# Optimization experiments

Hardware: AMD Instinct MI355X
Metric: run time of the kernel (lower is better)

The kernel has to match this reference:

```python
import jax, jax.numpy as jnp
import numpy as np

N_PER_GRAPH = 1000   # nodes per graph block (shape of A)
N_GRAPHS = 100       # number of block-diagonal replicas
N = N_PER_GRAPH * N_GRAPHS  # total nodes = 100000
HIDDEN = 128
DEG = 8
E = N * DEG          # total edges = 800000
LN_EPS = 1e-5


def setup_inputs() -> dict:
    key = jax.random.key(0)
    kx, kr, kc, kw, kb = jax.random.split(key, 5)
    # x rows: [S(N); I(N); R(N); params(N)] with beta in col0, gamma in col1
    x = jax.random.normal(kx, (4 * N, HIDDEN), dtype=jnp.float32)
    # block-diagonal COO edges: indices within each graph offset by graph id * n
    offs = jnp.repeat(jnp.arange(N_GRAPHS, dtype=jnp.int64) * N_PER_GRAPH,
                      N_PER_GRAPH * DEG)
    edge_row = offs + jax.random.randint(kr, (E,), 0, N_PER_GRAPH, dtype=jnp.int64)
    edge_col = offs + jax.random.randint(kc, (E,), 0, N_PER_GRAPH, dtype=jnp.int64)
    W = jax.random.normal(kw, (HIDDEN, HIDDEN), dtype=jnp.float32)
    b = jax.random.normal(kb, (HIDDEN,), dtype=jnp.float32)
    ln_w = jnp.ones((HIDDEN,), dtype=jnp.float32)
    ln_b = jnp.zeros((HIDDEN,), dtype=jnp.float32)
    t = jax.random.uniform(jax.random.fold_in(key, 7), (1,), dtype=jnp.float32)
    return {"t": t, "x": x, "edge_row": edge_row, "edge_col": edge_col,
            "W": W, "b": b, "ln_w": ln_w, "ln_b": ln_b}


def reference(t, x, edge_row, edge_col, W, b, ln_w, ln_b):
    n4 = x.shape[0]
    n = n4 // 4
    sir = x[: 3 * n]                       # [3N, H]
    beta = x[3 * n :, 0]                   # [N]
    gam = x[3 * n :, 1]                    # [N]
    h = jax.nn.relu(sir @ W.T + b)         # Linear + ReLU
    S, I, R = h[:n], h[n : 2 * n], h[2 * n :]
    # block-diagonal adjacency aggregation: AI[row] += I[col]
    AI = jax.ops.segment_sum(I[edge_col], edge_row, num_segments=n)
    dS = -beta[:, None] * (AI * S)
    dI = -dS - gam[:, None] * I
    dR = gam[:, None] * I

    def ln(v):
        m = jnp.mean(v, axis=-1, keepdims=True)
        var = jnp.mean(jnp.square(v - m), axis=-1, keepdims=True)
        return (v - m) * jax.lax.rsqrt(var + LN_EPS) * ln_w + ln_b

    return jnp.concatenate([ln(dS), ln(dI), ln(dR), x[3 * n :]], axis=0)
```

## Files before the change

### kernel.cpp

```cpp
#include <hip/hip_runtime.h>

#define HID 128
#define NPG 1000
#define NGRAPH 100
#define NNODES (NPG * NGRAPH)
#define DEG 8
#define LN_EPS 1e-5f

#define K1_ROWS 128

typedef _Float16 half8 __attribute__((ext_vector_type(8)));
typedef float f32x4 __attribute__((ext_vector_type(4)));

__device__ inline void cvt_split(const float4 a, const float4 b,
                                 half8& hi, half8& lo)
{
    float v[8] = {a.x, a.y, a.z, a.w, b.x, b.y, b.z, b.w};
    #pragma unroll
    for (int i = 0; i < 8; ++i) {
        _Float16 h = (_Float16)v[i];
        hi[i] = h;
        lo[i] = (_Float16)(v[i] - (float)h);
    }
}

__global__ __launch_bounds__(256, 2) void k_gemm_relu(
    const float* __restrict__ x, const float* __restrict__ W,
    const float* __restrict__ bias, float* __restrict__ h, int nrows)
{
    __shared__ alignas(16) _Float16 Xh[K1_ROWS * 64];
    __shared__ alignas(16) _Float16 Xl[K1_ROWS * 64];
    __shared__ alignas(16) _Float16 Wh[HID * 64];
    __shared__ alignas(16) _Float16 Wl[HID * 64];

    const int tid  = threadIdx.x;
    const int lane = tid & 63;
    const int w    = tid >> 6;
    const int wr   = (w >> 1) * 64;
    const int wc   = (w & 1) * 64;
    const int r0   = blockIdx.x * K1_ROWS;

    f32x4 acc[4][4];
    #pragma unroll
    for (int i = 0; i < 4; ++i)
        #pragma unroll
        for (int j = 0; j < 4; ++j)
            acc[i][j] = (f32x4){0.f, 0.f, 0.f, 0.f};

    const int l15 = lane & 15;
    const int lg  = lane >> 4;
    const int swz = (lane & 7) << 3;

    for (int kh = 0; kh < 2; ++kh) {
        if (kh) __syncthreads();

        #pragma unroll
        for (int it = 0; it < 4; ++it) {
            int chunk = tid + it * 256;
            int row = chunk >> 3, kg = chunk & 7;
            const float* gp = &x[(size_t)(r0 + row) * HID + kh * 64 + kg * 8];
            float4 a = reinterpret_cast<const float4*>(gp)[0];
            float4 b = reinterpret_cast<const float4*>(gp)[1];
            half8 hi, lo; cvt_split(a, b, hi, lo);
            int widx = (row * 64 + kg * 8) ^ ((row & 7) << 3);
            *reinterpret_cast<half8*>(&Xh[widx]) = hi;
            *reinterpret_cast<half8*>(&Xl[widx]) = lo;
        }
        #pragma unroll
        for (int it = 0; it < 4; ++it) {
            int chunk = tid + it * 256;
            int row = chunk >> 3, kg = chunk & 7;
            const float* gp = &W[(size_t)row * HID + kh * 64 + kg * 8];
            float4 a = reinterpret_cast<const float4*>(gp)[0];
            float4 b = reinterpret_cast<const float4*>(gp)[1];
            half8 hi, lo; cvt_split(a, b, hi, lo);
            int widx = (row * 64 + kg * 8) ^ ((row & 7) << 3);
            *reinterpret_cast<half8*>(&Wh[widx]) = hi;
            *reinterpret_cast<half8*>(&Wl[widx]) = lo;
        }
        __syncthreads();

        #pragma unroll
        for (int kb = 0; kb < 2; ++kb) {
            half8 ah[4], al[4], bh[4], bl[4];
            #pragma unroll
            for (int t = 0; t < 4; ++t) {
                int arow = wr + t * 16 + l15;
                int aidx = (arow * 64 + kb * 32 + lg * 8) ^ swz;
                ah[t] = *reinterpret_cast<const half8*>(&Xh[aidx]);
                al[t] = *reinterpret_cast<const half8*>(&Xl[aidx]);
                int bcol = wc + t * 16 + l15;
                int bidx = (bcol * 64 + kb * 32 + lg * 8) ^ swz;
                bh[t] = *reinterpret_cast<const half8*>(&Wh[bidx]);
                bl[t] = *reinterpret_cast<const half8*>(&Wl[bidx]);
            }
            #pragma unroll
            for (int rt = 0; rt < 4; ++rt)
                #pragma unroll
                for (int ct = 0; ct < 4; ++ct) {
                    acc[rt][ct] = __builtin_amdgcn_mfma_f32_16x16x32_f16(
                        ah[rt], bh[ct], acc[rt][ct], 0, 0, 0);
                    acc[rt][ct] = __builtin_amdgcn_mfma_f32_16x16x32_f16(
                        al[rt], bh[ct], acc[rt][ct], 0, 0, 0);
                    acc[rt][ct] = __builtin_amdgcn_mfma_f32_16x16x32_f16(
                        ah[rt], bl[ct], acc[rt][ct], 0, 0, 0);
                }
        }
    }

    float bc[4];
    #pragma unroll
    for (int ct = 0; ct < 4; ++ct) bc[ct] = bias[wc + ct * 16 + l15];

    #pragma unroll
    for (int rt = 0; rt < 4; ++rt) {
        int rowb = r0 + wr + rt * 16 + lg * 4;
        #pragma unroll
        for (int j = 0; j < 4; ++j) {
            if (rowb + j < nrows) {
                float* hp = &h[(size_t)(rowb + j) * HID + wc + l15];
                #pragma unroll
                for (int ct = 0; ct < 4; ++ct)
                    hp[ct * 16] = fmaxf(acc[rt][ct][j] + bc[ct], 0.f);
            }
        }
    }
}

#define BPG  8
#define RPB  (NPG / BPG)
#define ECAP 1280

__global__ __launch_bounds__(256) void k_aggregate(
    const float* __restrict__ I, const int* __restrict__ erow,
    const int* __restrict__ ecol, float* __restrict__ AI)
{
    __shared__ int cnt[RPB];
    __shared__ int wp[RPB];
    __shared__ int scan[256];
    __shared__ int cols[ECAP];

    const int g     = blockIdx.x / BPG;
    const int q     = blockIdx.x % BPG;
    const int row0  = q * RPB;
    const int nbase = g * NPG;
    const int ebase = g * (NPG * DEG);
    const int tid   = threadIdx.x;

    if (tid < RPB) cnt[tid] = 0;
    __syncthreads();

    for (int e = tid; e < NPG * DEG; e += 256) {
        int rl = erow[ebase + e] - nbase - row0;
        if ((unsigned)rl < (unsigned)RPB) atomicAdd(&cnt[rl], 1);
    }
    __syncthreads();

    int v = (tid < RPB) ? cnt[tid] : 0;
    scan[tid] = v;
    __syncthreads();
    #pragma unroll
    for (int s = 1; s < 256; s <<= 1) {
        int t = (tid >= s) ? scan[tid - s] : 0;
        __syncthreads();
        scan[tid] += t;
        __syncthreads();
    }
    if (tid < RPB) wp[tid] = scan[tid] - cnt[tid];
    __syncthreads();

    for (int e = tid; e < NPG * DEG; e += 256) {
        int rl = erow[ebase + e] - nbase - row0;
        if ((unsigned)rl < (unsigned)RPB) {
            int p = atomicAdd(&wp[rl], 1);
            if (p < ECAP) cols[p] = ecol[ebase + e];
        }
    }
    __syncthreads();

    const int wave = tid >> 6, lane = tid & 63;
    const int c = lane * 2;
    for (int n = wave; n < RPB; n += 4) {
        int deg = cnt[n];
        int end = wp[n];
        int j   = end - deg;
        float ax = 0.f, ay = 0.f;
        for (; j + 4 <= end; j += 4) {
            int c0 = cols[j], c1 = cols[j + 1], c2 = cols[j + 2], c3 = cols[j + 3];
            float2 v0 = *reinterpret_cast<const float2*>(&I[(size_t)c0 * HID + c]);
            float2 v1 = *reinterpret_cast<const float2*>(&I[(size_t)c1 * HID + c]);
            float2 v2 = *reinterpret_cast<const float2*>(&I[(size_t)c2 * HID + c]);
            float2 v3 = *reinterpret_cast<const float2*>(&I[(size_t)c3 * HID + c]);
            ax += v0.x + v1.x + v2.x + v3.x;
            ay += v0.y + v1.y + v2.y + v3.y;
        }
        for (; j < end; j++) {
            float2 v0 = *reinterpret_cast<const float2*>(&I[(size_t)cols[j] * HID + c]);
            ax += v0.x; ay += v0.y;
        }
        float2 o; o.x = ax; o.y = ay;
        *reinterpret_cast<float2*>(&AI[(size_t)(nbase + row0 + n) * HID + c]) = o;
    }
}

__global__ __launch_bounds__(256) void k_final(
    const float* __restrict__ x, const float* __restrict__ lnw,
    const float* __restrict__ lnb, float* __restrict__ out)
{
    const int wave = threadIdx.x >> 6;
    const int lane = threadIdx.x & 63;
    const size_t i = (size_t)blockIdx.x * 4 + wave;
    const int c    = lane * 2;
    const size_t N = NNODES;

    float2 S  = *reinterpret_cast<const float2*>(&out[i * HID + c]);
    float2 I2 = *reinterpret_cast<const float2*>(&out[(N + i) * HID + c]);
    float2 A  = *reinterpret_cast<const float2*>(&out[(2 * N + i) * HID + c]);

    const float beta = x[(3 * N + i) * HID + 0];
    const float gam  = x[(3 * N + i) * HID + 1];

    float2 dS, dI, dR;
    dS.x = -beta * (A.x * S.x);
    dS.y = -beta * (A.y * S.y);
    dI.x = -dS.x - gam * I2.x;
    dI.y = -dS.y - gam * I2.y;
    dR.x = gam * I2.x;
    dR.y = gam * I2.y;

    const float2 lw = *reinterpret_cast<const float2*>(&lnw[c]);
    const float2 lb = *reinterpret_cast<const float2*>(&lnb[c]);

    auto ln_store = [&](float2 v, float* dst) {
        float s = v.x + v.y;
        #pragma unroll
        for (int m = 1; m < 64; m <<= 1) s += __shfl_xor(s, m);
        const float mean = s * (1.f / 128.f);
        const float dx = v.x - mean, dy = v.y - mean;
        float q = dx * dx + dy * dy;
        #pragma unroll
        for (int m = 1; m < 64; m <<= 1) q += __shfl_xor(q, m);
        const float rs = rsqrtf(q * (1.f / 128.f) + LN_EPS);
        float2 o;
        o.x = dx * rs * lw.x + lb.x;
        o.y = dy * rs * lw.y + lb.y;
        *reinterpret_cast<float2*>(dst) = o;
    };

    ln_store(dS, &out[i * HID + c]);
    ln_store(dI, &out[(N + i) * HID + c]);
    ln_store(dR, &out[(2 * N + i) * HID + c]);

    const float2 t2 =
        *reinterpret_cast<const float2*>(&x[(3 * N + i) * HID + c]);
    *reinterpret_cast<float2*>(&out[(3 * N + i) * HID + c]) = t2;
}

extern "C" void kernel_launch(void* const* d_in, const int* in_sizes, int n_in,
                              void* d_out, int out_size, void* d_ws,
                              size_t ws_size, hipStream_t stream)
{
    const float* x   = (const float*)d_in[1];
    const int* erow  = (const int*)d_in[2];
    const int* ecol  = (const int*)d_in[3];
    const float* W   = (const float*)d_in[4];
    const float* b   = (const float*)d_in[5];
    const float* lnw = (const float*)d_in[6];
    const float* lnb = (const float*)d_in[7];
    float* out = (float*)d_out;

    float* Iptr  = out + (size_t)NNODES * HID;
    float* AIptr = out + (size_t)2 * NNODES * HID;

    const int nrows = 2 * NNODES;
    k_gemm_relu<<<(nrows + K1_ROWS - 1) / K1_ROWS, 256, 0, stream>>>(
        x, W, b, out, nrows);
    k_aggregate<<<NGRAPH * BPG, 256, 0, stream>>>(Iptr, erow, ecol, AIptr);
    k_final<<<NNODES / 4, 256, 0, stream>>>(x, lnw, lnb, out);
}
```

Baseline: 489.0 us.

## Fuse neighbor aggregation with SIR update and LayerNorm, stage I in workspace

The GEMM kernel now writes the I activations to a separate workspace buffer and S into the output. A single new kernel then builds the per-block CSR, gathers neighbor I rows, computes dS/dI/dR, layer-normalizes them and writes all four output sections. This removes the AI intermediate round trip through global memory and one kernel launch. In exchange, the per-node elementwise and LayerNorm work now runs inside the gather kernel's limited 800-block grid. It also depends on the workspace being large enough, with the old three-kernel path kept as a fallback.

```diff
diff --git a/kernel.cpp b/kernel.cpp
--- a/kernel.cpp
+++ b/kernel.cpp
@@ -26,7 +26,8 @@
 
 __global__ __launch_bounds__(256, 2) void k_gemm_relu(
     const float* __restrict__ x, const float* __restrict__ W,
-    const float* __restrict__ bias, float* __restrict__ h, int nrows)
+    const float* __restrict__ bias, float* __restrict__ outS,
+    float* __restrict__ outI, int nrows)
 {
     __shared__ alignas(16) _Float16 Xh[K1_ROWS * 64];
     __shared__ alignas(16) _Float16 Xl[K1_ROWS * 64];
@@ -117,8 +118,12 @@
         int rowb = r0 + wr + rt * 16 + lg * 4;
         #pragma unroll
         for (int j = 0; j < 4; ++j) {
-            if (rowb + j < nrows) {
-                float* hp = &h[(size_t)(rowb + j) * HID + wc + l15];
+            int r = rowb + j;
+            if (r < nrows) {
+                float* base = (r < NNODES)
+                                  ? &outS[(size_t)r * HID]
+                                  : &outI[(size_t)(r - NNODES) * HID];
+                float* hp = base + wc + l15;
                 #pragma unroll
                 for (int ct = 0; ct < 4; ++ct)
                     hp[ct * 16] = fmaxf(acc[rt][ct][j] + bc[ct], 0.f);
@@ -130,6 +135,121 @@
 #define BPG  8
 #define RPB  (NPG / BPG)
 #define ECAP 1280
+
+__global__ __launch_bounds__(256) void k_agg_final(
+    const float* __restrict__ x, const float* __restrict__ Sbuf,
+    const float* __restrict__ Ibuf, const int* __restrict__ erow,
+    const int* __restrict__ ecol, const float* __restrict__ lnw,
+    const float* __restrict__ lnb, float* __restrict__ out)
+{
+    __shared__ int cnt[RPB];
+    __shared__ int wp[RPB];
+    __shared__ int scan[256];
+    __shared__ int cols[ECAP];
+
+    const int g     = blockIdx.x / BPG;
+    const int q     = blockIdx.x % BPG;
+    const int row0  = q * RPB;
+    const int nbase = g * NPG;
+    const int ebase = g * (NPG * DEG);
+    const int tid   = threadIdx.x;
+
+    if (tid < RPB) cnt[tid] = 0;
+    __syncthreads();
+
+    for (int e = tid; e < NPG * DEG; e += 256) {
+        int rl = erow[ebase + e] - nbase - row0;
+        if ((unsigned)rl < (unsigned)RPB) atomicAdd(&cnt[rl], 1);
+    }
+    __syncthreads();
+
+    int v = (tid < RPB) ? cnt[tid] : 0;
+    scan[tid] = v;
+    __syncthreads();
+    #pragma unroll
+    for (int s = 1; s < 256; s <<= 1) {
+        int t = (tid >= s) ? scan[tid - s] : 0;
+        __syncthreads();
+        scan[tid] += t;
+        __syncthreads();
+    }
+    if (tid < RPB) wp[tid] = scan[tid] - cnt[tid];
+    __syncthreads();
+
+    for (int e = tid; e < NPG * DEG; e += 256) {
+        int rl = erow[ebase + e] - nbase - row0;
+        if ((unsigned)rl < (unsigned)RPB) {
+            int p = atomicAdd(&wp[rl], 1);
+            if (p < ECAP) cols[p] = ecol[ebase + e];
+        }
+    }
+    __syncthreads();
+
+    const int wave = tid >> 6, lane = tid & 63;
+    const int c = lane * 2;
+    const size_t N = NNODES;
+
+    const float2 lw = *reinterpret_cast<const float2*>(&lnw[c]);
+    const float2 lb = *reinterpret_cast<const float2*>(&lnb[c]);
+
+    auto ln_store = [&](float2 vv, float* dst) {
+        float s = vv.x + vv.y;
+        #pragma unroll
+        for (int m = 1; m < 64; m <<= 1) s += __shfl_xor(s, m);
+        const float mean = s * (1.f / 128.f);
+        const float dx = vv.x - mean, dy = vv.y - mean;
+        float qq = dx * dx + dy * dy;
+        #pragma unroll
+        for (int m = 1; m < 64; m <<= 1) qq += __shfl_xor(qq, m);
+        const float rs = rsqrtf(qq * (1.f / 128.f) + LN_EPS);
+        float2 o;
+        o.x = dx * rs * lw.x + lb.x;
+        o.y = dy * rs * lw.y + lb.y;
+        *reinterpret_cast<float2*>(dst) = o;
+    };
+
+    for (int n = wave; n < RPB; n += 4) {
+        const size_t gn = (size_t)(nbase + row0 + n);
+
+        float2 Sv = *reinterpret_cast<const float2*>(&Sbuf[gn * HID + c]);
+        float2 Iv = *reinterpret_cast<const float2*>(&Ibuf[gn * HID + c]);
+        float2 T  = *reinterpret_cast<const float2*>(&x[(3 * N + gn) * HID + c]);
+
+        int deg = cnt[n];
+        int end = wp[n];
+        int j   = end - deg;
+        float ax = 0.f, ay = 0.f;
+        for (; j + 4 <= end; j += 4) {
+            int c0 = cols[j], c1 = cols[j + 1], c2 = cols[j + 2], c3 = cols[j + 3];
+            float2 v0 = *reinterpret_cast<const float2*>(&Ibuf[(size_t)c0 * HID + c]);
+            float2 v1 = *reinterpret_cast<const float2*>(&Ibuf[(size_t)c1 * HID + c]);
+            float2 v2 = *reinterpret_cast<const float2*>(&Ibuf[(size_t)c2 * HID + c]);
+            float2 v3 = *reinterpret_cast<const float2*>(&Ibuf[(size_t)c3 * HID + c]);
+            ax += v0.x + v1.x + v2.x + v3.x;
+            ay += v0.y + v1.y + v2.y + v3.y;
+        }
+        for (; j < end; j++) {
+            float2 v0 = *reinterpret_cast<const float2*>(&Ibuf[(size_t)cols[j] * HID + c]);
+            ax += v0.x; ay += v0.y;
+        }
+
+        const float beta = __shfl(T.x, 0);
+        const float gam  = __shfl(T.y, 0);
+
+        float2 dS, dI, dR;
+        dS.x = -beta * (ax * Sv.x);
+        dS.y = -beta * (ay * Sv.y);
+        dI.x = -dS.x - gam * Iv.x;
+        dI.y = -dS.y - gam * Iv.y;
+        dR.x = gam * Iv.x;
+        dR.y = gam * Iv.y;
+
+        ln_store(dS, &out[gn * HID + c]);
+        ln_store(dI, &out[(N + gn) * HID + c]);
+        ln_store(dR, &out[(2 * N + gn) * HID + c]);
+        *reinterpret_cast<float2*>(&out[(3 * N + gn) * HID + c]) = T;
+    }
+}
 
 __global__ __launch_bounds__(256) void k_aggregate(
     const float* __restrict__ I, const int* __restrict__ erow,
@@ -269,12 +389,21 @@
     const float* lnb = (const float*)d_in[7];
     float* out = (float*)d_out;
 
-    float* Iptr  = out + (size_t)NNODES * HID;
-    float* AIptr = out + (size_t)2 * NNODES * HID;
-
     const int nrows = 2 * NNODES;
-    k_gemm_relu<<<(nrows + K1_ROWS - 1) / K1_ROWS, 256, 0, stream>>>(
-        x, W, b, out, nrows);
-    k_aggregate<<<NGRAPH * BPG, 256, 0, stream>>>(Iptr, erow, ecol, AIptr);
-    k_final<<<NNODES / 4, 256, 0, stream>>>(x, lnw, lnb, out);
-}
+    const size_t ineed = (size_t)NNODES * HID * sizeof(float);
+
+    if (d_ws != nullptr && ws_size >= ineed) {
+        float* Iws = (float*)d_ws;
+        k_gemm_relu<<<(nrows + K1_ROWS - 1) / K1_ROWS, 256, 0, stream>>>(
+            x, W, b, out, Iws, nrows);
+        k_agg_final<<<NGRAPH * BPG, 256, 0, stream>>>(
+            x, out, Iws, erow, ecol, lnw, lnb, out);
+    } else {
+        float* Iptr  = out + (size_t)NNODES * HID;
+        float* AIptr = out + (size_t)2 * NNODES * HID;
+        k_gemm_relu<<<(nrows + K1_ROWS - 1) / K1_ROWS, 256, 0, stream>>>(
+            x, W, b, out, Iptr, nrows);
+        k_aggregate<<<NGRAPH * BPG, 256, 0, stream>>>(Iptr, erow, ecol, AIptr);
+        k_final<<<NNODES / 4, 256, 0, stream>>>(x, lnw, lnb, out);
+    }
+}
```

After: 493.9 us. About the same (+1.0%).

## Build per-row adjacency lists with atomics and fuse gather with LayerNorm

Applied to the files above, without the earlier changes.

Adds a path that writes I into a workspace buffer and builds per-node edge lists inside the output rows with atomic slot counters. A new kernel then fuses the neighbour gather, the SIR update and the three LayerNorms, one node per half-wave. This replaces the per-graph shared-memory aggregation kernel and its separate AI write and read-back. Edge order within a row is nondeterministic, rows with more than 64 edges are silently truncated, and the path depends on workspace being available.

```diff
diff --git a/kernel.cpp b/kernel.cpp
--- a/kernel.cpp
+++ b/kernel.cpp
@@ -26,7 +26,8 @@
 
 __global__ __launch_bounds__(256, 2) void k_gemm_relu(
     const float* __restrict__ x, const float* __restrict__ W,
-    const float* __restrict__ bias, float* __restrict__ h, int nrows)
+    const float* __restrict__ bias, float* __restrict__ outS,
+    float* __restrict__ outI, float* __restrict__ csr_base, int nrows)
 {
     __shared__ alignas(16) _Float16 Xh[K1_ROWS * 64];
     __shared__ alignas(16) _Float16 Xl[K1_ROWS * 64];
@@ -39,6 +40,12 @@
     const int wr   = (w >> 1) * 64;
     const int wc   = (w & 1) * 64;
     const int r0   = blockIdx.x * K1_ROWS;
+
+    if (csr_base != nullptr) {
+        int nid = blockIdx.x * 256 + tid;
+        if (nid < NNODES)
+            *reinterpret_cast<int*>(&csr_base[(size_t)nid * HID]) = 0;
+    }
 
     f32x4 acc[4][4];
     #pragma unroll
@@ -117,14 +124,156 @@
         int rowb = r0 + wr + rt * 16 + lg * 4;
         #pragma unroll
         for (int j = 0; j < 4; ++j) {
-            if (rowb + j < nrows) {
-                float* hp = &h[(size_t)(rowb + j) * HID + wc + l15];
+            int r = rowb + j;
+            if (r < nrows) {
+                float* base = (r < NNODES)
+                                  ? &outS[(size_t)r * HID]
+                                  : &outI[(size_t)(r - NNODES) * HID];
+                float* hp = base + wc + l15;
                 #pragma unroll
                 for (int ct = 0; ct < 4; ++ct)
                     hp[ct * 16] = fmaxf(acc[rt][ct][j] + bc[ct], 0.f);
             }
         }
     }
+}
+
+__global__ __launch_bounds__(256) void k_edges(
+    const int* __restrict__ erow, const int* __restrict__ ecol,
+    float* __restrict__ csr_base)
+{
+    const int e4 = (blockIdx.x * 256 + threadIdx.x) * 4;
+    if (e4 >= NNODES * DEG) return;
+    int4 rr = *reinterpret_cast<const int4*>(&erow[e4]);
+    int4 cc = *reinterpret_cast<const int4*>(&ecol[e4]);
+    #pragma unroll
+    for (int u = 0; u < 4; ++u) {
+        int r = (u == 0) ? rr.x : (u == 1) ? rr.y : (u == 2) ? rr.z : rr.w;
+        int c = (u == 0) ? cc.x : (u == 1) ? cc.y : (u == 2) ? cc.z : cc.w;
+        unsigned* cnt = reinterpret_cast<unsigned*>(&csr_base[(size_t)r * HID]);
+        unsigned slot = atomicAdd(cnt, 1u);
+        if (slot < 64u) reinterpret_cast<int*>(cnt)[4 + slot] = (int)c;
+    }
+}
+
+__global__ __launch_bounds__(256, 8) void k_gather_ln(
+    const float* __restrict__ x, const float* __restrict__ Ibuf,
+    const float* __restrict__ lnw, const float* __restrict__ lnb,
+    float* __restrict__ out)
+{
+    const int bi   = blockIdx.x;
+    const int xcd  = bi & 7, slt = bi >> 3;
+    const int id   = ((xcd < 4) ? xcd * 1563 : 4 * 1563 + (xcd - 4) * 1562) + slt;
+
+    const int tid  = threadIdx.x;
+    const int wave = tid >> 6, lane = tid & 63;
+    const int h    = lane >> 5;
+    const int l32  = lane & 31;
+    const int c4   = l32 * 4;
+    const size_t N = NNODES;
+    const size_t gn = (size_t)id * 8 + wave * 2 + h;
+
+    const int* csr = reinterpret_cast<const int*>(&out[(2 * N + gn) * HID]);
+
+    int  cntw = csr[0];
+    int4 ch0  = *reinterpret_cast<const int4*>(&csr[4]);
+    int4 ch1  = *reinterpret_cast<const int4*>(&csr[8]);
+    float4 Sv = *reinterpret_cast<const float4*>(&out[gn * HID + c4]);
+    float4 Iv = *reinterpret_cast<const float4*>(&Ibuf[gn * HID + c4]);
+    float4 T  = *reinterpret_cast<const float4*>(&x[(3 * N + gn) * HID + c4]);
+
+    const int deg = min(cntw, 64);
+
+    float ax = 0.f, ay = 0.f, az = 0.f, aw = 0.f;
+
+    auto proc = [&](int4 cc, int j) {
+        int  i0 = (j + 0 < deg) ? cc.x : 0;  float w0 = (j + 0 < deg) ? 1.f : 0.f;
+        int  i1 = (j + 1 < deg) ? cc.y : 0;  float w1 = (j + 1 < deg) ? 1.f : 0.f;
+        int  i2 = (j + 2 < deg) ? cc.z : 0;  float w2 = (j + 2 < deg) ? 1.f : 0.f;
+        int  i3 = (j + 3 < deg) ? cc.w : 0;  float w3 = (j + 3 < deg) ? 1.f : 0.f;
+        float4 v0 = *reinterpret_cast<const float4*>(&Ibuf[(size_t)i0 * HID + c4]);
+        float4 v1 = *reinterpret_cast<const float4*>(&Ibuf[(size_t)i1 * HID + c4]);
+        float4 v2 = *reinterpret_cast<const float4*>(&Ibuf[(size_t)i2 * HID + c4]);
+        float4 v3 = *reinterpret_cast<const float4*>(&Ibuf[(size_t)i3 * HID + c4]);
+        ax += w0 * v0.x + w1 * v1.x + w2 * v2.x + w3 * v3.x;
+        ay += w0 * v0.y + w1 * v1.y + w2 * v2.y + w3 * v3.y;
+        az += w0 * v0.z + w1 * v1.z + w2 * v2.z + w3 * v3.z;
+        aw += w0 * v0.w + w1 * v1.w + w2 * v2.w + w3 * v3.w;
+    };
+
+    if (deg > 0) proc(ch0, 0);
+    if (deg > 4) proc(ch1, 4);
+    #pragma unroll 1
+    for (int j = 8; j < deg; j += 4) {
+        int4 cc = *reinterpret_cast<const int4*>(&csr[4 + j]);
+        proc(cc, j);
+    }
+
+    const float beta = __shfl(T.x, h << 5);
+    const float gam  = __shfl(T.y, h << 5);
+
+    float4 dS, dI, dR;
+    dS.x = -beta * (ax * Sv.x);
+    dS.y = -beta * (ay * Sv.y);
+    dS.z = -beta * (az * Sv.z);
+    dS.w = -beta * (aw * Sv.w);
+    dI.x = -dS.x - gam * Iv.x;
+    dI.y = -dS.y - gam * Iv.y;
+    dI.z = -dS.z - gam * Iv.z;
+    dI.w = -dS.w - gam * Iv.w;
+    dR.x = gam * Iv.x;
+    dR.y = gam * Iv.y;
+    dR.z = gam * Iv.z;
+    dR.w = gam * Iv.w;
+
+    const float4 lwv = *reinterpret_cast<const float4*>(&lnw[c4]);
+    const float4 lbv = *reinterpret_cast<const float4*>(&lnb[c4]);
+
+    float sA = dS.x + dS.y + dS.z + dS.w;
+    float sB = dI.x + dI.y + dI.z + dI.w;
+    float sC = dR.x + dR.y + dR.z + dR.w;
+    #pragma unroll
+    for (int m = 1; m < 32; m <<= 1) {
+        sA += __shfl_xor(sA, m);
+        sB += __shfl_xor(sB, m);
+        sC += __shfl_xor(sC, m);
+    }
+    const float mA = sA * (1.f / 128.f);
+    const float mB = sB * (1.f / 128.f);
+    const float mC = sC * (1.f / 128.f);
+    float qA = (dS.x-mA)*(dS.x-mA) + (dS.y-mA)*(dS.y-mA)
+             + (dS.z-mA)*(dS.z-mA) + (dS.w-mA)*(dS.w-mA);
+    float qB = (dI.x-mB)*(dI.x-mB) + (dI.y-mB)*(dI.y-mB)
+             + (dI.z-mB)*(dI.z-mB) + (dI.w-mB)*(dI.w-mB);
+    float qC = (dR.x-mC)*(dR.x-mC) + (dR.y-mC)*(dR.y-mC)
+             + (dR.z-mC)*(dR.z-mC) + (dR.w-mC)*(dR.w-mC);
+    #pragma unroll
+    for (int m = 1; m < 32; m <<= 1) {
+        qA += __shfl_xor(qA, m);
+        qB += __shfl_xor(qB, m);
+        qC += __shfl_xor(qC, m);
+    }
+    const float rsA = rsqrtf(qA * (1.f / 128.f) + LN_EPS);
+    const float rsB = rsqrtf(qB * (1.f / 128.f) + LN_EPS);
+    const float rsC = rsqrtf(qC * (1.f / 128.f) + LN_EPS);
+
+    float4 o;
+    o.x = (dS.x - mA) * rsA * lwv.x + lbv.x;
+    o.y = (dS.y - mA) * rsA * lwv.y + lbv.y;
+    o.z = (dS.z - mA) * rsA * lwv.z + lbv.z;
+    o.w = (dS.w - mA) * rsA * lwv.w + lbv.w;
+    *reinterpret_cast<float4*>(&out[gn * HID + c4]) = o;
+    o.x = (dI.x - mB) * rsB * lwv.x + lbv.x;
+    o.y = (dI.y - mB) * rsB * lwv.y + lbv.y;
+    o.z = (dI.z - mB) * rsB * lwv.z + lbv.z;
+    o.w = (dI.w - mB) * rsB * lwv.w + lbv.w;
+    *reinterpret_cast<float4*>(&out[(N + gn) * HID + c4]) = o;
+    o.x = (dR.x - mC) * rsC * lwv.x + lbv.x;
+    o.y = (dR.y - mC) * rsC * lwv.y + lbv.y;
+    o.z = (dR.z - mC) * rsC * lwv.z + lbv.z;
+    o.w = (dR.w - mC) * rsC * lwv.w + lbv.w;
+    *reinterpret_cast<float4*>(&out[(2 * N + gn) * HID + c4]) = o;
+    *reinterpret_cast<float4*>(&out[(3 * N + gn) * HID + c4]) = T;
 }
 
 #define BPG  8
@@ -269,12 +418,24 @@
     const float* lnb = (const float*)d_in[7];
     float* out = (float*)d_out;
 
-    float* Iptr  = out + (size_t)NNODES * HID;
-    float* AIptr = out + (size_t)2 * NNODES * HID;
-
     const int nrows = 2 * NNODES;
-    k_gemm_relu<<<(nrows + K1_ROWS - 1) / K1_ROWS, 256, 0, stream>>>(
-        x, W, b, out, nrows);
-    k_aggregate<<<NGRAPH * BPG, 256, 0, stream>>>(Iptr, erow, ecol, AIptr);
-    k_final<<<NNODES / 4, 256, 0, stream>>>(x, lnw, lnb, out);
-}
+    const size_t ineed = (size_t)NNODES * HID * sizeof(float);
+
+    if (d_ws != nullptr && ws_size >= ineed) {
+        float* Iws = (float*)d_ws;
+        float* csr = out + (size_t)2 * NNODES * HID;
+        k_gemm_relu<<<(nrows + K1_ROWS - 1) / K1_ROWS, 256, 0, stream>>>(
+            x, W, b, out, Iws, csr, nrows);
+        k_edges<<<(NNODES * DEG / 4 + 255) / 256, 256, 0, stream>>>(
+            erow, ecol, csr);
+        k_gather_ln<<<NNODES / 8, 256, 0, stream>>>(
+            x, Iws, lnw, lnb, out);
+    } else {
+        float* Iptr  = out + (size_t)NNODES * HID;
+        float* AIptr = out + (size_t)2 * NNODES * HID;
+        k_gemm_relu<<<(nrows + K1_ROWS - 1) / K1_ROWS, 256, 0, stream>>>(
+            x, W, b, out, Iptr, nullptr, nrows);
+        k_aggregate<<<NGRAPH * BPG, 256, 0, stream>>>(Iptr, erow, ecol, AIptr);
+        k_final<<<NNODES / 4, 256, 0, stream>>>(x, lnw, lnb, out);
+    }
+}
```

Result: faster. 476.1 us (-2.6%).
